# Kernel tuning notes

Measured on AMD Instinct MI355X. Metric: run time of the kernel, lower is better.

Reference implementation:

```python
import jax, jax.numpy as jnp
import numpy as np

N_NODES = 4096
N_EDGES = 32768
IN_FEAT = 256
OUT_FEAT = 128
HID = 64
IN_HEAD = 64
OUT_HEAD = 5
NEG_SLOPE = 0.2
EPS = 1e-16


def setup_inputs() -> dict:
    key = jax.random.key(0)
    ks = jax.random.split(key, 12)
    x = jax.random.normal(ks[0], (N_NODES, IN_FEAT), dtype=jnp.float32)
    src = jax.random.randint(ks[1], (N_EDGES,), 0, N_NODES)
    dst = jax.random.randint(ks[2], (N_EDGES,), 0, N_NODES)
    edge_index = jnp.stack([src, dst]).astype(jnp.int64)
    s1 = 1.0 / np.sqrt(IN_FEAT)
    s2 = 1.0 / np.sqrt(HID * IN_HEAD)
    W1 = jax.random.normal(ks[3], (IN_FEAT, IN_HEAD * HID), dtype=jnp.float32) * s1
    att_src1 = jax.random.normal(ks[4], (IN_HEAD, HID), dtype=jnp.float32) * 0.1
    att_dst1 = jax.random.normal(ks[5], (IN_HEAD, HID), dtype=jnp.float32) * 0.1
    b1 = jnp.zeros((IN_HEAD * HID,), dtype=jnp.float32)
    W2 = jax.random.normal(ks[6], (IN_HEAD * HID, OUT_HEAD * OUT_FEAT), dtype=jnp.float32) * s2
    att_src2 = jax.random.normal(ks[7], (OUT_HEAD, OUT_FEAT), dtype=jnp.float32) * 0.1
    att_dst2 = jax.random.normal(ks[8], (OUT_HEAD, OUT_FEAT), dtype=jnp.float32) * 0.1
    b2 = jnp.zeros((OUT_FEAT,), dtype=jnp.float32)
    return {"x": x, "edge_index": edge_index, "W1": W1, "att_src1": att_src1,
            "att_dst1": att_dst1, "b1": b1, "W2": W2, "att_src2": att_src2,
            "att_dst2": att_dst2, "b2": b2}


def _gat_conv(x, W, att_src, att_dst, bias, src, dst, heads, out_c, concat):
    # x: [N, F_in]; returns [N, heads*out_c] (concat) or [N, out_c] (mean)
    n = x.shape[0]
    h = (x @ W).reshape(n, heads, out_c)                       # [N,H,C]
    a_src = jnp.sum(h * att_src, axis=-1)                      # [N,H]
    a_dst = jnp.sum(h * att_dst, axis=-1)                      # [N,H]
    e = jax.nn.leaky_relu(a_src[src] + a_dst[dst], NEG_SLOPE)  # [E,H]
    # segment softmax over edges grouped by destination node (PyG softmax)
    m = jax.ops.segment_max(e, dst, num_segments=n)            # [N,H]
    ex = jnp.exp(e - m[dst])
    denom = jax.ops.segment_sum(ex, dst, num_segments=n)       # [N,H]
    alpha = ex / (denom[dst] + EPS)                            # [E,H]
    out = jax.ops.segment_sum(alpha[:, :, None] * h[src], dst, num_segments=n)  # [N,H,C]
    out = out.reshape(n, heads * out_c) if concat else out.mean(axis=1)
    return out + bias


def reference(x, edge_index, W1, att_src1, att_dst1, b1, W2, att_src2, att_dst2, b2):
    n = x.shape[0]
    # PyG GATConv default: add self loops
    loop = jnp.arange(n, dtype=edge_index.dtype)
    src = jnp.concatenate([edge_index[0], loop])
    dst = jnp.concatenate([edge_index[1], loop])
    # dropout layers are identity in eval mode
    h = _gat_conv(x, W1, att_src1, att_dst1, b1, src, dst, IN_HEAD, HID, True)
    h = jax.nn.elu(h)
    h = _gat_conv(h, W2, att_src2, att_dst2, b2, src, dst, OUT_HEAD, OUT_FEAT, False)
    s = jnp.mean(h, axis=0)
    return jnp.tanh(s)
```

## Files before the change

### kernel.cpp

```cpp
#include <hip/hip_runtime.h>
#include <hip/hip_bf16.h>

#define N_NODES 4096
#define NE      32768
#define E_TOT   (NE + N_NODES)
#define IN_FEAT 256
#define HID     64
#define IN_HEAD 64
#define F1      4096
#define OUT_HEAD 5
#define OUT_FEAT 128
#define F2      640
#define NEG_SLOPE 0.2f
#define EPS_A   1e-16f

typedef __bf16 bf16;
typedef bf16 bf16x8 __attribute__((ext_vector_type(8)));
typedef bf16 bf16x4 __attribute__((ext_vector_type(4)));
typedef float f32x4 __attribute__((ext_vector_type(4)));

__device__ inline void async_cp16(bf16* lds, const bf16* g) {
    __builtin_amdgcn_global_load_lds(
        (const __attribute__((address_space(1))) unsigned int*)g,
        (__attribute__((address_space(3))) unsigned int*)lds, 16, 0, 0);
}

__global__ void hist_kernel(const int* __restrict__ edst, int* counts) {
    int e = blockIdx.x * 256 + threadIdx.x;
    if (e >= E_TOT) return;
    int d = (e < NE) ? edst[e] : (e - NE);
    atomicAdd(&counts[d], 1);
}

__global__ void scan_kernel(const int* __restrict__ counts,
                            int* __restrict__ row_start, int* __restrict__ cursor) {
    __shared__ int part[256];
    __shared__ int pre[257];
    int t = threadIdx.x;
    int base = t * 16;
    int local[16];
    int s = 0;
#pragma unroll
    for (int i = 0; i < 16; ++i) { local[i] = s; s += counts[base + i]; }
    part[t] = s;
    __syncthreads();
    if (t == 0) {
        int r = 0;
        for (int i = 0; i < 256; ++i) { pre[i] = r; r += part[i]; }
        pre[256] = r;
    }
    __syncthreads();
    int off = pre[t];
#pragma unroll
    for (int i = 0; i < 16; ++i) {
        int v = off + local[i];
        row_start[base + i] = v;
        cursor[base + i] = v;
    }
    if (t == 0) row_start[N_NODES] = pre[256];
}

__global__ void scatter_kernel(const int* __restrict__ edst,
                               int* cursor, int* __restrict__ elist) {
    int e = blockIdx.x * 256 + threadIdx.x;
    if (e >= E_TOT) return;
    int d = (e < NE) ? edst[e] : (e - NE);
    int slot = atomicAdd(&cursor[d], 1);
    elist[slot] = e;
}

#define PB_X   512
#define PB_W1  1024
#define PB_W2  2560
__global__ __launch_bounds__(256)
void prep_kernel(const float* __restrict__ x, bf16* __restrict__ xb,
                 const float* __restrict__ W1, bf16* __restrict__ W1T,
                 const float* __restrict__ W2, bf16* __restrict__ W2T,
                 const float* __restrict__ as1, const float* __restrict__ ad1,
                 bf16* __restrict__ w1s, bf16* __restrict__ w1d) {
    __shared__ float tile[32][33];
    int b = blockIdx.x, t = threadIdx.x;
    if (b < PB_X) {
        int i = b * 256 + t;
        f32x4 a = *(const f32x4*)(x + (size_t)i * 8);
        f32x4 c = *(const f32x4*)(x + (size_t)i * 8 + 4);
        bf16x8 r;
        r[0] = (bf16)a[0]; r[1] = (bf16)a[1]; r[2] = (bf16)a[2]; r[3] = (bf16)a[3];
        r[4] = (bf16)c[0]; r[5] = (bf16)c[1]; r[6] = (bf16)c[2]; r[7] = (bf16)c[3];
        *(bf16x8*)(xb + (size_t)i * 8) = r;
    } else if (b < PB_X + PB_W1 + PB_W2) {
        const float* S; bf16* D; int R, C, gx, gy;
        if (b < PB_X + PB_W1) {
            int bb = b - PB_X;
            S = W1; D = W1T; R = IN_FEAT; C = F1;
            gx = bb % (F1 / 32); gy = bb / (F1 / 32);
        } else {
            int bb = b - PB_X - PB_W1;
            S = W2; D = W2T; R = F1; C = F2;
            gx = bb % (F2 / 32); gy = bb / (F2 / 32);
        }
        int tx = t & 31, ty = t >> 5;
        int c0 = gx * 32, r0 = gy * 32;
#pragma unroll
        for (int i = 0; i < 4; ++i)
            tile[ty + i * 8][tx] = S[(size_t)(r0 + ty + i * 8) * C + c0 + tx];
        __syncthreads();
#pragma unroll
        for (int i = 0; i < 4; ++i)
            D[(size_t)(c0 + ty + i * 8) * R + r0 + tx] = (bf16)tile[tx][ty + i * 8];
    } else {
        int id = (b - PB_X - PB_W1 - PB_W2) * 256 + t;
        int k = id >> 6, h = id & 63;
        const float* wrow = W1 + (size_t)k * F1 + h * HID;
        const float* a1 = as1 + h * HID;
        const float* a2 = ad1 + h * HID;
        float s = 0.f, d = 0.f;
#pragma unroll 8
        for (int c = 0; c < HID; ++c) {
            float w = wrow[c];
            s += w * a1[c];
            d += w * a2[c];
        }
        w1s[id] = (bf16)s;
        w1d[id] = (bf16)d;
    }
}

template <int SPLITK, bool SWZ, typename TC>
__global__ __launch_bounds__(256)
void gemm128_kernel(const bf16* __restrict__ A, const bf16* __restrict__ BT,
                    TC* __restrict__ C, int M, int N, int K) {
    __shared__ bf16 As[128][64];
    __shared__ bf16 Bs[128][64];
    const int tid  = threadIdx.x;
    const int wave = tid >> 6, lane = tid & 63;
    const int quad = lane >> 4, lr = lane & 15;
    int nb, mb, zb;
    if constexpr (SWZ) {
        int bid = blockIdx.x;
        int xx = bid & 7, q = bid >> 3;
        int gp = q / 5; nb = q - gp * 5;
        int g = gp * 8 + xx;
        mb = g >> 2; zb = g & 3;
    } else {
        nb = blockIdx.x; mb = blockIdx.y; zb = blockIdx.z;
    }
    const int m0 = mb * 128, n0 = nb * 128;
    const int kchunk = K / SPLITK;
    const int kbeg = zb * kchunk;
    const int wm = (wave >> 1) * 64;
    const int wn = (wave & 1) * 64;
    TC* Cz = C + (size_t)zb * M * N;

    const int srow = lane >> 3;
    const int scol = ((lane & 7) ^ srow) * 8;
    const int xk = lr & 7;

    f32x4 acc[4][4] = {};

    for (int kk = 0; kk < kchunk; kk += 64) {
        int k0 = kbeg + kk;
#pragma unroll
        for (int c = 0; c < 4; ++c) {
            int r = wave * 32 + c * 8;
            async_cp16(&As[r][0], A + (size_t)(m0 + r + srow) * K + k0 + scol);
            async_cp16(&Bs[r][0], BT + (size_t)(n0 + r + srow) * K + k0 + scol);
        }
        __syncthreads();

#pragma unroll
        for (int ks = 0; ks < 2; ++ks) {
            int ch = ((ks * 4 + quad) ^ xk) * 8;
            bf16x8 af[4], bfr[4];
#pragma unroll
            for (int mt = 0; mt < 4; ++mt)
                af[mt] = *(const bf16x8*)(&As[wm + mt * 16 + lr][ch]);
#pragma unroll
            for (int nt = 0; nt < 4; ++nt)
                bfr[nt] = *(const bf16x8*)(&Bs[wn + nt * 16 + lr][ch]);
#pragma unroll
            for (int mt = 0; mt < 4; ++mt)
#pragma unroll
                for (int nt = 0; nt < 4; ++nt)
                    acc[mt][nt] = __builtin_amdgcn_mfma_f32_16x16x32_bf16(
                        af[mt], bfr[nt], acc[mt][nt], 0, 0, 0);
        }
        __syncthreads();
    }

#pragma unroll
    for (int mt = 0; mt < 4; ++mt)
#pragma unroll
        for (int nt = 0; nt < 4; ++nt) {
            int row0 = m0 + wm + mt * 16 + quad * 4;
            int col = n0 + wn + nt * 16 + lr;
#pragma unroll
            for (int r = 0; r < 4; ++r)
                Cz[(size_t)(row0 + r) * N + col] = (TC)acc[mt][nt][r];
        }
}

__global__ __launch_bounds__(256)
void gemv1_kernel(const float* __restrict__ x,
                  const bf16* __restrict__ w1s, const bf16* __restrict__ w1d,
                  float* __restrict__ a_src, float* __restrict__ a_dst) {
    int wave = threadIdx.x >> 6, lane = threadIdx.x & 63;
    int n = blockIdx.x * 4 + wave;
    const float* xr = x + (size_t)n * IN_FEAT;
    float s = 0.f, d = 0.f;
    for (int k0 = 0; k0 < IN_FEAT; k0 += 4) {
        f32x4 xv = *(const f32x4*)(xr + k0);
#pragma unroll
        for (int j = 0; j < 4; ++j) {
            float xs = xv[j];
            s += xs * (float)w1s[(k0 + j) * IN_HEAD + lane];
            d += xs * (float)w1d[(k0 + j) * IN_HEAD + lane];
        }
    }
    a_src[n * IN_HEAD + lane] = s;
    a_dst[n * IN_HEAD + lane] = d;
}

__global__ __launch_bounds__(64)
void agg1_kernel(const int* __restrict__ es, const int* __restrict__ row_start,
                 const int* __restrict__ elist,
                 const float* __restrict__ a_src, const float* __restrict__ a_dst,
                 const bf16* __restrict__ H1, const float* __restrict__ b1,
                 bf16* __restrict__ h_elu) {
    int bid = blockIdx.x;
    int c = bid & 7;
    int d = bid >> 3;
    int lane = threadIdx.x;
    int gh = c * 8 + (lane >> 3);
    int sub = lane & 7;
    int beg = row_start[d], deg = row_start[d + 1] - beg;
    float adst = a_dst[d * IN_HEAD + gh];

    float m = -1e30f, den = 0.f;
    for (int i = sub; i < deg; i += 8) {
        int e = elist[beg + i];
        int s = (e < NE) ? es[e] : d;
        float l = a_src[s * IN_HEAD + gh] + adst;
        l = l > 0.f ? l : NEG_SLOPE * l;
        if (l > m) { den = den * __expf(m - l) + 1.f; m = l; }
        else den += __expf(l - m);
    }
#pragma unroll
    for (int o = 1; o <= 4; o <<= 1) {
        float mo = __shfl_xor(m, o);
        float dno = __shfl_xor(den, o);
        float mn = fmaxf(m, mo);
        den = den * __expf(m - mn) + dno * __expf(mo - mn);
        m = mn;
    }
    float dinv = 1.f / (den + EPS_A);

    int fbase = c * 512 + lane * 8;
    float acc[8] = {};
    for (int i = 0; i < deg; ++i) {
        int e = elist[beg + i];
        int s = (e < NE) ? es[e] : d;
        float l = a_src[s * IN_HEAD + gh] + adst;
        l = l > 0.f ? l : NEG_SLOPE * l;
        float alpha = __expf(l - m) * dinv;
        bf16x8 v = *(const bf16x8*)(H1 + (size_t)s * F1 + fbase);
#pragma unroll
        for (int j = 0; j < 8; ++j) acc[j] += alpha * (float)v[j];
    }

    bf16x8 o;
#pragma unroll
    for (int j = 0; j < 8; ++j) {
        float v = acc[j] + b1[fbase + j];
        o[j] = (bf16)(v > 0.f ? v : (__expf(v) - 1.f));
    }
    *(bf16x8*)(h_elu + (size_t)d * F1 + fbase) = o;
}

__global__ __launch_bounds__(192)
void fold2_kernel(const bf16* __restrict__ Hp,
                  const float* __restrict__ as2, const float* __restrict__ ad2,
                  float* __restrict__ H2,
                  float* __restrict__ a_src, float* __restrict__ a_dst) {
    int n = blockIdx.x, t = threadIdx.x;
    if (t >= 160) return;
    int h = t >> 5;
    f32x4 sum = {};
#pragma unroll
    for (int z = 0; z < 4; ++z) {
        bf16x4 v = *(const bf16x4*)(Hp + (size_t)z * N_NODES * F2 + (size_t)n * F2 + t * 4);
        sum[0] += (float)v[0]; sum[1] += (float)v[1];
        sum[2] += (float)v[2]; sum[3] += (float)v[3];
    }
    *(f32x4*)(H2 + (size_t)n * F2 + t * 4) = sum;
    f32x4 ws = *(const f32x4*)(as2 + t * 4);
    f32x4 wd = *(const f32x4*)(ad2 + t * 4);
    float s = sum[0] * ws[0] + sum[1] * ws[1] + sum[2] * ws[2] + sum[3] * ws[3];
    float d = sum[0] * wd[0] + sum[1] * wd[1] + sum[2] * wd[2] + sum[3] * wd[3];
#pragma unroll
    for (int o = 1; o <= 16; o <<= 1) {
        s += __shfl_xor(s, o);
        d += __shfl_xor(d, o);
    }
    if ((t & 31) == 0) {
        a_src[n * OUT_HEAD + h] = s;
        a_dst[n * OUT_HEAD + h] = d;
    }
}

__global__ void stats2_kernel(const int* __restrict__ es,
                              const int* __restrict__ row_start,
                              const int* __restrict__ elist,
                              const float* __restrict__ a_src,
                              const float* __restrict__ a_dst,
                              float* __restrict__ m2, float* __restrict__ dinv2) {
    int id = blockIdx.x * 256 + threadIdx.x;
    if (id >= N_NODES * OUT_HEAD) return;
    int d = id / OUT_HEAD, h = id - d * OUT_HEAD;
    int beg = row_start[d], deg = row_start[d + 1] - beg;
    float adst = a_dst[id];
    float m = -1e30f, den = 0.f;
    for (int i = 0; i < deg; ++i) {
        int e = elist[beg + i];
        int s = (e < NE) ? es[e] : d;
        float l = a_src[s * OUT_HEAD + h] + adst;
        l = l > 0.f ? l : NEG_SLOPE * l;
        if (l > m) { den = den * __expf(m - l) + 1.f; m = l; }
        else den += __expf(l - m);
    }
    m2[id] = m;
    dinv2[id] = 1.f / (den + EPS_A);
}

__global__ void beta_kernel(const int* __restrict__ es, const int* __restrict__ ed,
                            const float* __restrict__ a_src, const float* __restrict__ a_dst,
                            const float* __restrict__ m2, const float* __restrict__ dinv2,
                            float* __restrict__ beta) {
    int id = blockIdx.x * 256 + threadIdx.x;
    if (id >= E_TOT * OUT_HEAD) return;
    int e = id / OUT_HEAD, h = id - e * OUT_HEAD;
    int s = (e < NE) ? es[e] : (e - NE);
    int d = (e < NE) ? ed[e] : (e - NE);
    float l = a_src[s * OUT_HEAD + h] + a_dst[d * OUT_HEAD + h];
    l = l > 0.f ? l : NEG_SLOPE * l;
    float alpha = __expf(l - m2[d * OUT_HEAD + h]) * dinv2[d * OUT_HEAD + h];
    atomicAdd(&beta[s * OUT_HEAD + h], alpha);
}

__global__ __launch_bounds__(256)
void wsum_kernel(const float* __restrict__ H2, const float* __restrict__ beta,
                 float* __restrict__ acc_out) {
    __shared__ float buf[F2];
    int t = threadIdx.x;
    int n0 = blockIdx.x * 32;
    int h = t >> 5;
    float a0 = 0.f, a1 = 0.f, a2 = 0.f, a3 = 0.f;
    if (t < 160) {
        for (int i = 0; i < 32; ++i) {
            int s = n0 + i;
            float bh = beta[s * OUT_HEAD + h];
            f32x4 v = *(const f32x4*)(H2 + (size_t)s * F2 + t * 4);
            a0 += bh * v[0]; a1 += bh * v[1];
            a2 += bh * v[2]; a3 += bh * v[3];
        }
        buf[t * 4 + 0] = a0; buf[t * 4 + 1] = a1;
        buf[t * 4 + 2] = a2; buf[t * 4 + 3] = a3;
    }
    __syncthreads();
    if (t < OUT_FEAT) {
        float s = 0.f;
#pragma unroll
        for (int hh = 0; hh < OUT_HEAD; ++hh) s += buf[hh * OUT_FEAT + t];
        atomicAdd(&acc_out[(blockIdx.x & 7) * OUT_FEAT + t], s);
    }
}

__global__ void tanh_kernel(const float* __restrict__ acc_out,
                            const float* __restrict__ b2, float* __restrict__ out) {
    int c = threadIdx.x;
    float tot = 0.f;
#pragma unroll
    for (int k = 0; k < 8; ++k) tot += acc_out[k * OUT_FEAT + c];
    out[c] = tanhf(tot * (1.f / (OUT_HEAD * (float)N_NODES)) + b2[c]);
}

extern "C" void kernel_launch(void* const* d_in, const int* in_sizes, int n_in,
                              void* d_out, int out_size, void* d_ws, size_t ws_size,
                              hipStream_t stream) {
    const float* x        = (const float*)d_in[0];
    const int*   ei       = (const int*)d_in[1];
    const float* W1       = (const float*)d_in[2];
    const float* att_src1 = (const float*)d_in[3];
    const float* att_dst1 = (const float*)d_in[4];
    const float* b1       = (const float*)d_in[5];
    const float* W2       = (const float*)d_in[6];
    const float* att_src2 = (const float*)d_in[7];
    const float* att_dst2 = (const float*)d_in[8];
    const float* b2       = (const float*)d_in[9];
    float* out = (float*)d_out;

    const int* esrc = ei;
    const int* edst = ei + NE;

    char* p = (char*)d_ws;
    auto bump = [&](size_t bytes) {
        void* r = (void*)p;
        p += (bytes + 255) & ~(size_t)255;
        return r;
    };
    bf16*  H1     = (bf16*)bump((size_t)N_NODES * F1 * 2);
    bf16*  h_elu  = (bf16*)bump((size_t)N_NODES * F1 * 2);
    float* H2     = (float*)bump((size_t)N_NODES * F2 * 4);
    bf16*  xb     = (bf16*)bump((size_t)N_NODES * IN_FEAT * 2);
    bf16*  W1T    = (bf16*)bump((size_t)F1 * IN_FEAT * 2);
    bf16*  W2T    = (bf16*)bump((size_t)F2 * F1 * 2);
    bf16*  w1s    = (bf16*)bump((size_t)IN_FEAT * IN_HEAD * 2);
    bf16*  w1d    = (bf16*)bump((size_t)IN_FEAT * IN_HEAD * 2);
    float* a_src1 = (float*)bump((size_t)N_NODES * IN_HEAD * 4);
    float* a_dst1 = (float*)bump((size_t)N_NODES * IN_HEAD * 4);
    float* a_src2 = (float*)bump((size_t)N_NODES * OUT_HEAD * 4);
    float* a_dst2 = (float*)bump((size_t)N_NODES * OUT_HEAD * 4);
    float* m2     = (float*)bump((size_t)N_NODES * OUT_HEAD * 4);
    float* dinv2  = (float*)bump((size_t)N_NODES * OUT_HEAD * 4);
    int*   row_start = (int*)bump((N_NODES + 1) * 4);
    int*   cursor = (int*)bump(N_NODES * 4);
    int*   elist  = (int*)bump(E_TOT * 4);
    int*   counts = (int*)bump(N_NODES * 4 + N_NODES * OUT_HEAD * 4 + 8 * OUT_FEAT * 4);
    float* beta    = (float*)((char*)counts + N_NODES * 4);
    float* acc_out = beta + N_NODES * OUT_HEAD;
    bf16* Hp = H1;

    hipMemsetAsync(counts, 0,
                   N_NODES * 4 + N_NODES * OUT_HEAD * 4 + 8 * OUT_FEAT * 4, stream);

    hist_kernel<<<(E_TOT + 255) / 256, 256, 0, stream>>>(edst, counts);
    scan_kernel<<<1, 256, 0, stream>>>(counts, row_start, cursor);
    scatter_kernel<<<(E_TOT + 255) / 256, 256, 0, stream>>>(edst, cursor, elist);

    prep_kernel<<<PB_X + PB_W1 + PB_W2 + 64, 256, 0, stream>>>(
        x, xb, W1, W1T, W2, W2T, att_src1, att_dst1, w1s, w1d);

    gemm128_kernel<1, false, bf16>
        <<<dim3(F1 / 128, N_NODES / 128, 1), 256, 0, stream>>>(
        xb, W1T, H1, N_NODES, F1, IN_FEAT);
    gemv1_kernel<<<N_NODES / 4, 256, 0, stream>>>(x, w1s, w1d, a_src1, a_dst1);
    agg1_kernel<<<N_NODES * 8, 64, 0, stream>>>(
        esrc, row_start, elist, a_src1, a_dst1, H1, b1, h_elu);

    gemm128_kernel<4, true, bf16><<<640, 256, 0, stream>>>(
        h_elu, W2T, Hp, N_NODES, F2, F1);
    fold2_kernel<<<N_NODES, 192, 0, stream>>>(
        Hp, att_src2, att_dst2, H2, a_src2, a_dst2);
    stats2_kernel<<<(N_NODES * OUT_HEAD + 255) / 256, 256, 0, stream>>>(
        esrc, row_start, elist, a_src2, a_dst2, m2, dinv2);
    beta_kernel<<<(E_TOT * OUT_HEAD + 255) / 256, 256, 0, stream>>>(
        esrc, edst, a_src2, a_dst2, m2, dinv2, beta);
    wsum_kernel<<<N_NODES / 32, 256, 0, stream>>>(H2, beta, acc_out);

    tanh_kernel<<<1, OUT_FEAT, 0, stream>>>(acc_out, b2, out);
}
```

Before: 245.3 us.

## Merge independent kernels into phase kernels to cut launch count

Folds the histogram into the prep kernel and puts the CSR scatter, layer-1 GEMM and attention GEMV into one combined launch using block-range dispatch. Stats and beta computation are merged so each destination thread replays its edges and does the beta atomics itself. The final tanh reduction moves into wsum through a last-block-done counter. The aim is fewer kernel launches and better overlap of small independent stages, at the cost of shared-memory footprint for all blocks and a serial per-destination edge loop.

```diff
diff --git a/kernel.cpp b/kernel.cpp
--- a/kernel.cpp
+++ b/kernel.cpp
@@ -25,61 +25,85 @@
         (__attribute__((address_space(3))) unsigned int*)lds, 16, 0, 0);
 }
 
-__global__ void hist_kernel(const int* __restrict__ edst, int* counts) {
-    int e = blockIdx.x * 256 + threadIdx.x;
-    if (e >= E_TOT) return;
-    int d = (e < NE) ? edst[e] : (e - NE);
-    atomicAdd(&counts[d], 1);
-}
-
-__global__ void scan_kernel(const int* __restrict__ counts,
-                            int* __restrict__ row_start, int* __restrict__ cursor) {
-    __shared__ int part[256];
-    __shared__ int pre[257];
-    int t = threadIdx.x;
-    int base = t * 16;
-    int local[16];
-    int s = 0;
-#pragma unroll
-    for (int i = 0; i < 16; ++i) { local[i] = s; s += counts[base + i]; }
-    part[t] = s;
-    __syncthreads();
-    if (t == 0) {
-        int r = 0;
-        for (int i = 0; i < 256; ++i) { pre[i] = r; r += part[i]; }
-        pre[256] = r;
-    }
-    __syncthreads();
-    int off = pre[t];
-#pragma unroll
-    for (int i = 0; i < 16; ++i) {
-        int v = off + local[i];
-        row_start[base + i] = v;
-        cursor[base + i] = v;
-    }
-    if (t == 0) row_start[N_NODES] = pre[256];
-}
-
-__global__ void scatter_kernel(const int* __restrict__ edst,
-                               int* cursor, int* __restrict__ elist) {
-    int e = blockIdx.x * 256 + threadIdx.x;
-    if (e >= E_TOT) return;
-    int d = (e < NE) ? edst[e] : (e - NE);
-    int slot = atomicAdd(&cursor[d], 1);
-    elist[slot] = e;
-}
-
+template <typename TC>
+__device__ __forceinline__ void gemm_body(
+    const bf16* __restrict__ A, const bf16* __restrict__ BT, TC* __restrict__ Cz,
+    int m0, int n0, int kbeg, int kchunk, int Ncols, int Kdim,
+    bf16 (*As)[64], bf16 (*Bs)[64], int tid) {
+    const int wave = tid >> 6, lane = tid & 63;
+    const int quad = lane >> 4, lr = lane & 15;
+    const int wm = (wave >> 1) * 64;
+    const int wn = (wave & 1) * 64;
+    const int srow = lane >> 3;
+    const int scol = ((lane & 7) ^ srow) * 8;
+    const int xk = lr & 7;
+
+    f32x4 acc[4][4] = {};
+
+    for (int kk = 0; kk < kchunk; kk += 64) {
+        int k0 = kbeg + kk;
+#pragma unroll
+        for (int c = 0; c < 4; ++c) {
+            int r = wave * 32 + c * 8;
+            async_cp16(&As[r][0], A + (size_t)(m0 + r + srow) * Kdim + k0 + scol);
+            async_cp16(&Bs[r][0], BT + (size_t)(n0 + r + srow) * Kdim + k0 + scol);
+        }
+        __syncthreads();
+
+#pragma unroll
+        for (int ks = 0; ks < 2; ++ks) {
+            int ch = ((ks * 4 + quad) ^ xk) * 8;
+            bf16x8 af[4], bfr[4];
+#pragma unroll
+            for (int mt = 0; mt < 4; ++mt)
+                af[mt] = *(const bf16x8*)(&As[wm + mt * 16 + lr][ch]);
+#pragma unroll
+            for (int nt = 0; nt < 4; ++nt)
+                bfr[nt] = *(const bf16x8*)(&Bs[wn + nt * 16 + lr][ch]);
+#pragma unroll
+            for (int mt = 0; mt < 4; ++mt)
+#pragma unroll
+                for (int nt = 0; nt < 4; ++nt)
+                    acc[mt][nt] = __builtin_amdgcn_mfma_f32_16x16x32_bf16(
+                        af[mt], bfr[nt], acc[mt][nt], 0, 0, 0);
+        }
+        __syncthreads();
+    }
+
+#pragma unroll
+    for (int mt = 0; mt < 4; ++mt)
+#pragma unroll
+        for (int nt = 0; nt < 4; ++nt) {
+            int row0 = m0 + wm + mt * 16 + quad * 4;
+            int col = n0 + wn + nt * 16 + lr;
+#pragma unroll
+            for (int r = 0; r < 4; ++r)
+                Cz[(size_t)(row0 + r) * Ncols + col] = (TC)acc[mt][nt][r];
+        }
+}
+
+#define PB_H   144
 #define PB_X   512
 #define PB_W1  1024
 #define PB_W2  2560
 __global__ __launch_bounds__(256)
-void prep_kernel(const float* __restrict__ x, bf16* __restrict__ xb,
-                 const float* __restrict__ W1, bf16* __restrict__ W1T,
-                 const float* __restrict__ W2, bf16* __restrict__ W2T,
-                 const float* __restrict__ as1, const float* __restrict__ ad1,
-                 bf16* __restrict__ w1s, bf16* __restrict__ w1d) {
+void phaseA_kernel(const int* __restrict__ edst, int* __restrict__ counts,
+                   const float* __restrict__ x, bf16* __restrict__ xb,
+                   const float* __restrict__ W1, bf16* __restrict__ W1T,
+                   const float* __restrict__ W2, bf16* __restrict__ W2T,
+                   const float* __restrict__ as1, const float* __restrict__ ad1,
+                   bf16* __restrict__ w1s, bf16* __restrict__ w1d) {
     __shared__ float tile[32][33];
-    int b = blockIdx.x, t = threadIdx.x;
+    int b0 = blockIdx.x, t = threadIdx.x;
+    if (b0 < PB_H) {
+        int e = b0 * 256 + t;
+        if (e < E_TOT) {
+            int d = (e < NE) ? edst[e] : (e - NE);
+            atomicAdd(&counts[d], 1);
+        }
+        return;
+    }
+    int b = b0 - PB_H;
     if (b < PB_X) {
         int i = b * 256 + t;
         f32x4 a = *(const f32x4*)(x + (size_t)i * 8);
@@ -126,99 +150,78 @@
     }
 }
 
-template <int SPLITK, bool SWZ, typename TC>
+__global__ void scan_kernel(const int* __restrict__ counts,
+                            int* __restrict__ row_start, int* __restrict__ cursor) {
+    __shared__ int part[256];
+    __shared__ int pre[257];
+    int t = threadIdx.x;
+    int base = t * 16;
+    int local[16];
+    int s = 0;
+#pragma unroll
+    for (int i = 0; i < 16; ++i) { local[i] = s; s += counts[base + i]; }
+    part[t] = s;
+    __syncthreads();
+    if (t == 0) {
+        int r = 0;
+        for (int i = 0; i < 256; ++i) { pre[i] = r; r += part[i]; }
+        pre[256] = r;
+    }
+    __syncthreads();
+    int off = pre[t];
+#pragma unroll
+    for (int i = 0; i < 16; ++i) {
+        int v = off + local[i];
+        row_start[base + i] = v;
+        cursor[base + i] = v;
+    }
+    if (t == 0) row_start[N_NODES] = pre[256];
+}
+
+#define PC_S   144
+#define PC_G1  1024
 __global__ __launch_bounds__(256)
-void gemm128_kernel(const bf16* __restrict__ A, const bf16* __restrict__ BT,
-                    TC* __restrict__ C, int M, int N, int K) {
+void phaseC_kernel(const int* __restrict__ edst, int* cursor, int* __restrict__ elist,
+                   const bf16* __restrict__ xb, const bf16* __restrict__ W1T,
+                   bf16* __restrict__ H1,
+                   const float* __restrict__ x,
+                   const bf16* __restrict__ w1s, const bf16* __restrict__ w1d,
+                   float* __restrict__ a_src, float* __restrict__ a_dst) {
     __shared__ bf16 As[128][64];
     __shared__ bf16 Bs[128][64];
-    const int tid  = threadIdx.x;
-    const int wave = tid >> 6, lane = tid & 63;
-    const int quad = lane >> 4, lr = lane & 15;
-    int nb, mb, zb;
-    if constexpr (SWZ) {
-        int bid = blockIdx.x;
+    int b = blockIdx.x, t = threadIdx.x;
+    if (b < PC_S) {
+        int e = b * 256 + t;
+        if (e < E_TOT) {
+            int d = (e < NE) ? edst[e] : (e - NE);
+            int slot = atomicAdd(&cursor[d], 1);
+            elist[slot] = e;
+        }
+    } else if (b < PC_S + PC_G1) {
+        int bid = b - PC_S;
         int xx = bid & 7, q = bid >> 3;
-        int gp = q / 5; nb = q - gp * 5;
-        int g = gp * 8 + xx;
-        mb = g >> 2; zb = g & 3;
+        int mb = xx * 4 + (q >> 5);
+        int nb = q & 31;
+        gemm_body<bf16>(xb, W1T, H1, mb * 128, nb * 128, 0, IN_FEAT,
+                        F1, IN_FEAT, As, Bs, t);
     } else {
-        nb = blockIdx.x; mb = blockIdx.y; zb = blockIdx.z;
-    }
-    const int m0 = mb * 128, n0 = nb * 128;
-    const int kchunk = K / SPLITK;
-    const int kbeg = zb * kchunk;
-    const int wm = (wave >> 1) * 64;
-    const int wn = (wave & 1) * 64;
-    TC* Cz = C + (size_t)zb * M * N;
-
-    const int srow = lane >> 3;
-    const int scol = ((lane & 7) ^ srow) * 8;
-    const int xk = lr & 7;
-
-    f32x4 acc[4][4] = {};
-
-    for (int kk = 0; kk < kchunk; kk += 64) {
-        int k0 = kbeg + kk;
-#pragma unroll
-        for (int c = 0; c < 4; ++c) {
-            int r = wave * 32 + c * 8;
-            async_cp16(&As[r][0], A + (size_t)(m0 + r + srow) * K + k0 + scol);
-            async_cp16(&Bs[r][0], BT + (size_t)(n0 + r + srow) * K + k0 + scol);
-        }
-        __syncthreads();
-
-#pragma unroll
-        for (int ks = 0; ks < 2; ++ks) {
-            int ch = ((ks * 4 + quad) ^ xk) * 8;
-            bf16x8 af[4], bfr[4];
-#pragma unroll
-            for (int mt = 0; mt < 4; ++mt)
-                af[mt] = *(const bf16x8*)(&As[wm + mt * 16 + lr][ch]);
-#pragma unroll
-            for (int nt = 0; nt < 4; ++nt)
-                bfr[nt] = *(const bf16x8*)(&Bs[wn + nt * 16 + lr][ch]);
-#pragma unroll
-            for (int mt = 0; mt < 4; ++mt)
-#pragma unroll
-                for (int nt = 0; nt < 4; ++nt)
-                    acc[mt][nt] = __builtin_amdgcn_mfma_f32_16x16x32_bf16(
-                        af[mt], bfr[nt], acc[mt][nt], 0, 0, 0);
-        }
-        __syncthreads();
-    }
-
-#pragma unroll
-    for (int mt = 0; mt < 4; ++mt)
-#pragma unroll
-        for (int nt = 0; nt < 4; ++nt) {
-            int row0 = m0 + wm + mt * 16 + quad * 4;
-            int col = n0 + wn + nt * 16 + lr;
-#pragma unroll
-            for (int r = 0; r < 4; ++r)
-                Cz[(size_t)(row0 + r) * N + col] = (TC)acc[mt][nt][r];
-        }
-}
-
-__global__ __launch_bounds__(256)
-void gemv1_kernel(const float* __restrict__ x,
-                  const bf16* __restrict__ w1s, const bf16* __restrict__ w1d,
-                  float* __restrict__ a_src, float* __restrict__ a_dst) {
-    int wave = threadIdx.x >> 6, lane = threadIdx.x & 63;
-    int n = blockIdx.x * 4 + wave;
-    const float* xr = x + (size_t)n * IN_FEAT;
-    float s = 0.f, d = 0.f;
-    for (int k0 = 0; k0 < IN_FEAT; k0 += 4) {
-        f32x4 xv = *(const f32x4*)(xr + k0);
-#pragma unroll
-        for (int j = 0; j < 4; ++j) {
-            float xs = xv[j];
-            s += xs * (float)w1s[(k0 + j) * IN_HEAD + lane];
-            d += xs * (float)w1d[(k0 + j) * IN_HEAD + lane];
-        }
-    }
-    a_src[n * IN_HEAD + lane] = s;
-    a_dst[n * IN_HEAD + lane] = d;
+        int nblk = b - PC_S - PC_G1;
+        int wave = t >> 6, lane = t & 63;
+        int n = nblk * 4 + wave;
+        const float* xr = x + (size_t)n * IN_FEAT;
+        float s = 0.f, d = 0.f;
+        for (int k0 = 0; k0 < IN_FEAT; k0 += 4) {
+            f32x4 xv = *(const f32x4*)(xr + k0);
+#pragma unroll
+            for (int j = 0; j < 4; ++j) {
+                float xs = xv[j];
+                s += xs * (float)w1s[(k0 + j) * IN_HEAD + lane];
+                d += xs * (float)w1d[(k0 + j) * IN_HEAD + lane];
+            }
+        }
+        a_src[n * IN_HEAD + lane] = s;
+        a_dst[n * IN_HEAD + lane] = d;
+    }
 }
 
 __global__ __launch_bounds__(64)
@@ -257,6 +260,7 @@
 
     int fbase = c * 512 + lane * 8;
     float acc[8] = {};
+#pragma unroll 2
     for (int i = 0; i < deg; ++i) {
         int e = elist[beg + i];
         int s = (e < NE) ? es[e] : d;
@@ -275,6 +279,22 @@
         o[j] = (bf16)(v > 0.f ? v : (__expf(v) - 1.f));
     }
     *(bf16x8*)(h_elu + (size_t)d * F1 + fbase) = o;
+}
+
+__global__ __launch_bounds__(256)
+void gemm2_kernel(const bf16* __restrict__ A, const bf16* __restrict__ BT,
+                  bf16* __restrict__ C) {
+    __shared__ bf16 As[128][64];
+    __shared__ bf16 Bs[128][64];
+    int bid = blockIdx.x;
+    int xx = bid & 7, q = bid >> 3;
+    int gp = q / 5, nb = q - gp * 5;
+    int g = gp * 8 + xx;
+    int mb = g >> 2, zb = g & 3;
+    const int kchunk = F1 / 4;
+    gemm_body<bf16>(A, BT, C + (size_t)zb * N_NODES * F2,
+                    mb * 128, nb * 128, zb * kchunk, kchunk,
+                    F2, F1, As, Bs, threadIdx.x);
 }
 
 __global__ __launch_bounds__(192)
@@ -308,12 +328,12 @@
     }
 }
 
-__global__ void stats2_kernel(const int* __restrict__ es,
-                              const int* __restrict__ row_start,
-                              const int* __restrict__ elist,
-                              const float* __restrict__ a_src,
-                              const float* __restrict__ a_dst,
-                              float* __restrict__ m2, float* __restrict__ dinv2) {
+__global__ void statsbeta2_kernel(const int* __restrict__ es,
+                                  const int* __restrict__ row_start,
+                                  const int* __restrict__ elist,
+                                  const float* __restrict__ a_src,
+                                  const float* __restrict__ a_dst,
+                                  float* __restrict__ beta) {
     int id = blockIdx.x * 256 + threadIdx.x;
     if (id >= N_NODES * OUT_HEAD) return;
     int d = id / OUT_HEAD, h = id - d * OUT_HEAD;
@@ -328,29 +348,23 @@
         if (l > m) { den = den * __expf(m - l) + 1.f; m = l; }
         else den += __expf(l - m);
     }
-    m2[id] = m;
-    dinv2[id] = 1.f / (den + EPS_A);
-}
-
-__global__ void beta_kernel(const int* __restrict__ es, const int* __restrict__ ed,
-                            const float* __restrict__ a_src, const float* __restrict__ a_dst,
-                            const float* __restrict__ m2, const float* __restrict__ dinv2,
-                            float* __restrict__ beta) {
-    int id = blockIdx.x * 256 + threadIdx.x;
-    if (id >= E_TOT * OUT_HEAD) return;
-    int e = id / OUT_HEAD, h = id - e * OUT_HEAD;
-    int s = (e < NE) ? es[e] : (e - NE);
-    int d = (e < NE) ? ed[e] : (e - NE);
-    float l = a_src[s * OUT_HEAD + h] + a_dst[d * OUT_HEAD + h];
-    l = l > 0.f ? l : NEG_SLOPE * l;
-    float alpha = __expf(l - m2[d * OUT_HEAD + h]) * dinv2[d * OUT_HEAD + h];
-    atomicAdd(&beta[s * OUT_HEAD + h], alpha);
+    float dinv = 1.f / (den + EPS_A);
+    for (int i = 0; i < deg; ++i) {
+        int e = elist[beg + i];
+        int s = (e < NE) ? es[e] : d;
+        float l = a_src[s * OUT_HEAD + h] + adst;
+        l = l > 0.f ? l : NEG_SLOPE * l;
+        float alpha = __expf(l - m) * dinv;
+        atomicAdd(&beta[s * OUT_HEAD + h], alpha);
+    }
 }
 
 __global__ __launch_bounds__(256)
 void wsum_kernel(const float* __restrict__ H2, const float* __restrict__ beta,
-                 float* __restrict__ acc_out) {
+                 float* __restrict__ acc_out, int* __restrict__ done_ctr,
+                 const float* __restrict__ b2, float* __restrict__ out) {
     __shared__ float buf[F2];
+    __shared__ int lflag;
     int t = threadIdx.x;
     int n0 = blockIdx.x * 32;
     int h = t >> 5;
@@ -373,15 +387,18 @@
         for (int hh = 0; hh < OUT_HEAD; ++hh) s += buf[hh * OUT_FEAT + t];
         atomicAdd(&acc_out[(blockIdx.x & 7) * OUT_FEAT + t], s);
     }
-}
-
-__global__ void tanh_kernel(const float* __restrict__ acc_out,
-                            const float* __restrict__ b2, float* __restrict__ out) {
-    int c = threadIdx.x;
-    float tot = 0.f;
-#pragma unroll
-    for (int k = 0; k < 8; ++k) tot += acc_out[k * OUT_FEAT + c];
-    out[c] = tanhf(tot * (1.f / (OUT_HEAD * (float)N_NODES)) + b2[c]);
+    __threadfence();
+    __syncthreads();
+    if (t == 0) lflag = (atomicAdd(done_ctr, 1) == (N_NODES / 32) - 1);
+    __syncthreads();
+    if (lflag && t < OUT_FEAT) {
+        float tot = 0.f;
+#pragma unroll
+        for (int k = 0; k < 8; ++k)
+            tot += __hip_atomic_load(&acc_out[k * OUT_FEAT + t],
+                                     __ATOMIC_RELAXED, __HIP_MEMORY_SCOPE_AGENT);
+        out[t] = tanhf(tot * (1.f / (OUT_HEAD * (float)N_NODES)) + b2[t]);
+    }
 }
 
 extern "C" void kernel_launch(void* const* d_in, const int* in_sizes, int n_in,
@@ -420,42 +437,30 @@
     float* a_dst1 = (float*)bump((size_t)N_NODES * IN_HEAD * 4);
     float* a_src2 = (float*)bump((size_t)N_NODES * OUT_HEAD * 4);
     float* a_dst2 = (float*)bump((size_t)N_NODES * OUT_HEAD * 4);
-    float* m2     = (float*)bump((size_t)N_NODES * OUT_HEAD * 4);
-    float* dinv2  = (float*)bump((size_t)N_NODES * OUT_HEAD * 4);
     int*   row_start = (int*)bump((N_NODES + 1) * 4);
     int*   cursor = (int*)bump(N_NODES * 4);
     int*   elist  = (int*)bump(E_TOT * 4);
-    int*   counts = (int*)bump(N_NODES * 4 + N_NODES * OUT_HEAD * 4 + 8 * OUT_FEAT * 4);
+    size_t zbytes = N_NODES * 4 + N_NODES * OUT_HEAD * 4 + 8 * OUT_FEAT * 4 + 256;
+    int*   counts = (int*)bump(zbytes);
     float* beta    = (float*)((char*)counts + N_NODES * 4);
     float* acc_out = beta + N_NODES * OUT_HEAD;
+    int*   done_ctr = (int*)(acc_out + 8 * OUT_FEAT);
     bf16* Hp = H1;
 
-    hipMemsetAsync(counts, 0,
-                   N_NODES * 4 + N_NODES * OUT_HEAD * 4 + 8 * OUT_FEAT * 4, stream);
-
-    hist_kernel<<<(E_TOT + 255) / 256, 256, 0, stream>>>(edst, counts);
+    hipMemsetAsync(counts, 0, zbytes, stream);
+
+    phaseA_kernel<<<PB_H + PB_X + PB_W1 + PB_W2 + 64, 256, 0, stream>>>(
+        edst, counts, x, xb, W1, W1T, W2, W2T, att_src1, att_dst1, w1s, w1d);
     scan_kernel<<<1, 256, 0, stream>>>(counts, row_start, cursor);
-    scatter_kernel<<<(E_TOT + 255) / 256, 256, 0, stream>>>(edst, cursor, elist);
-
-    prep_kernel<<<PB_X + PB_W1 + PB_W2 + 64, 256, 0, stream>>>(
-        x, xb, W1, W1T, W2, W2T, att_src1, att_dst1, w1s, w1d);
-
-    gemm128_kernel<1, false, bf16>
-        <<<dim3(F1 / 128, N_NODES / 128, 1), 256, 0, stream>>>(
-        xb, W1T, H1, N_NODES, F1, IN_FEAT);
-    gemv1_kernel<<<N_NODES / 4, 256, 0, stream>>>(x, w1s, w1d, a_src1, a_dst1);
+    phaseC_kernel<<<PC_S + PC_G1 + N_NODES / 4, 256, 0, stream>>>(
+        edst, cursor, elist, xb, W1T, H1, x, w1s, w1d, a_src1, a_dst1);
     agg1_kernel<<<N_NODES * 8, 64, 0, stream>>>(
         esrc, row_start, elist, a_src1, a_dst1, H1, b1, h_elu);
-
-    gemm128_kernel<4, true, bf16><<<640, 256, 0, stream>>>(
-        h_elu, W2T, Hp, N_NODES, F2, F1);
+    gemm2_kernel<<<640, 256, 0, stream>>>(h_elu, W2T, Hp);
     fold2_kernel<<<N_NODES, 192, 0, stream>>>(
         Hp, att_src2, att_dst2, H2, a_src2, a_dst2);
-    stats2_kernel<<<(N_NODES * OUT_HEAD + 255) / 256, 256, 0, stream>>>(
-        esrc, row_start, elist, a_src2, a_dst2, m2, dinv2);
-    beta_kernel<<<(E_TOT * OUT_HEAD + 255) / 256, 256, 0, stream>>>(
-        esrc, edst, a_src2, a_dst2, m2, dinv2, beta);
-    wsum_kernel<<<N_NODES / 32, 256, 0, stream>>>(H2, beta, acc_out);
-
-    tanh_kernel<<<1, OUT_FEAT, 0, stream>>>(acc_out, b2, out);
-}
+    statsbeta2_kernel<<<(N_NODES * OUT_HEAD + 255) / 256, 256, 0, stream>>>(
+        esrc, row_start, elist, a_src2, a_dst2, beta);
+    wsum_kernel<<<N_NODES / 32, 256, 0, stream>>>(
+        H2, beta, acc_out, done_ctr, b2, out);
+}
```

New measurement: 256.4 us. 4.5% more time.
